# Kernel tuning notes

Measured on AMD Instinct MI355X. Metric: run time of the kernel, lower is better.

Reference implementation:

```python
import jax, jax.numpy as jnp
import numpy as np

BLOCK = 64  # bitsandbytes 4-bit blocksize
OUT, IN = 4096, 4096
# NF4 codebook (bitsandbytes values)
NF4_CODE = np.array([
    -1.0, -0.6961928009986877, -0.5250730514526367, -0.39491748809814453,
    -0.28444138169288635, -0.18477343022823334, -0.09105003625154495, 0.0,
    0.07958029955625534, 0.16093020141124725, 0.24611230194568634,
    0.33791524171829224, 0.44070982933044434, 0.5626170039176941,
    0.7229568362236023, 1.0], dtype=np.float32)


def setup_inputs() -> dict:
    key = jax.random.key(0)
    k1, k2, k3 = jax.random.split(key, 3)
    x = jax.random.normal(k1, (8, 2048, IN), dtype=jnp.float32)
    qweight = jax.random.randint(k2, (OUT * IN,), 0, 16, dtype=jnp.int32)
    absmax = jax.random.uniform(k3, (OUT * IN // BLOCK,), dtype=jnp.float32)
    return {"x": x, "qweight": qweight, "absmax": absmax}


def reference(x, qweight, absmax):
    code = jnp.asarray(NF4_CODE)
    # dequantize: codebook lookup, then per-block absmax scaling
    w = code[qweight].reshape(-1, BLOCK) * absmax[:, None]  # [n_blocks, BLOCK]
    W = w.reshape(OUT, IN)                                   # [out, in]
    # linear: y = x @ W^T  (no bias: quantized_bias is None)
    return jnp.einsum('bsi,oi->bso', x, W)
```

## Files before the change

### kernel.cpp

```cpp
#include <hip/hip_runtime.h>
#include <hip/hip_bf16.h>
#include <stdint.h>

#define IN_DIM  4096
#define OUT_DIM 4096
#define M_DIM   16384
#define BK      64
#define NT      (IN_DIM / BK)

typedef float f32x4 __attribute__((ext_vector_type(4)));
typedef short bf16x8 __attribute__((ext_vector_type(8)));
typedef short bf16x4 __attribute__((ext_vector_type(4)));
typedef int   i32x4 __attribute__((ext_vector_type(4)));

__device__ __constant__ float NF4_CODE_D[16] = {
    -1.0f, -0.6961928009986877f, -0.5250730514526367f, -0.39491748809814453f,
    -0.28444138169288635f, -0.18477343022823334f, -0.09105003625154495f, 0.0f,
    0.07958029955625534f, 0.16093020141124725f, 0.24611230194568634f,
    0.33791524171829224f, 0.44070982933044434f, 0.5626170039176941f,
    0.7229568362236023f, 1.0f};

static __device__ __forceinline__ ushort f2bf(float f) {
  union { float f; uint32_t u; } v; v.f = f;
  uint32_t r = v.u + 0x7FFFu + ((v.u >> 16) & 1u);
  return (ushort)(r >> 16);
}

#define NB_W 8192
__global__ void prep(const float* __restrict__ x, const int* __restrict__ q,
                     const float* __restrict__ am, ushort* __restrict__ xb,
                     ushort* __restrict__ w) {
  if (blockIdx.x < NB_W) {
    __shared__ float code[16];
    if (threadIdx.x < 16) code[threadIdx.x] = NF4_CODE_D[threadIdx.x];
    __syncthreads();
    size_t t = (size_t)blockIdx.x * 256 + threadIdx.x;
    size_t base = t * 8;
    i32x4 qa = *(const i32x4*)(q + base);
    i32x4 qb = *(const i32x4*)(q + base + 4);
    float s = am[base >> 6];
    bf16x8 o;
    o[0] = (short)f2bf(code[qa[0] & 15] * s);
    o[1] = (short)f2bf(code[qa[1] & 15] * s);
    o[2] = (short)f2bf(code[qa[2] & 15] * s);
    o[3] = (short)f2bf(code[qa[3] & 15] * s);
    o[4] = (short)f2bf(code[qb[0] & 15] * s);
    o[5] = (short)f2bf(code[qb[1] & 15] * s);
    o[6] = (short)f2bf(code[qb[2] & 15] * s);
    o[7] = (short)f2bf(code[qb[3] & 15] * s);
    *(bf16x8*)(w + base) = o;
  } else {
    size_t t = (size_t)(blockIdx.x - NB_W) * 256 + threadIdx.x;
    size_t base = t * 8;
    f32x4 a = *(const f32x4*)(x + base);
    f32x4 b = *(const f32x4*)(x + base + 4);
    bf16x8 o;
    o[0] = (short)f2bf(a[0]); o[1] = (short)f2bf(a[1]);
    o[2] = (short)f2bf(a[2]); o[3] = (short)f2bf(a[3]);
    o[4] = (short)f2bf(b[0]); o[5] = (short)f2bf(b[1]);
    o[6] = (short)f2bf(b[2]); o[7] = (short)f2bf(b[3]);
    *(bf16x8*)(xb + base) = o;
  }
}

static __device__ __forceinline__ void llds16(const ushort* g, ushort* l) {
  __builtin_amdgcn_global_load_lds(
      (const __attribute__((address_space(1))) void*)g,
      (__attribute__((address_space(3))) void*)l, 16, 0, 0);
}

__global__ __launch_bounds__(512, 2) void gemm256(const ushort* __restrict__ Xb,
                                                  const ushort* __restrict__ W,
                                                  float* __restrict__ Y) {
  __shared__ ushort As[2][256 * BK];
  __shared__ ushort Bs[2][256 * BK];

  const int tid  = threadIdx.x;
  const int lane = tid & 63;
  const int wid  = tid >> 6;
  const int wr   = wid >> 2;
  const int wc   = wid & 3;
  const int l15  = lane & 15;
  const int kg   = lane >> 4;
  const int l7   = lane & 7;

  const int bid = blockIdx.x;
  const int wg  = (bid & 7) * 128 + (bid >> 3);
  const int tm  = wg >> 4;
  const int tn  = wg & 15;
  const size_t row0 = (size_t)tm * 256;
  const size_t col0 = (size_t)tn * 256;

  const int srow  = tid >> 3;
  const int scol8 = ((tid & 7) ^ (srow & 7)) * 8;
  const int wbase = wid << 9;

  f32x4  acc[8][4] = {};
  bf16x8 aA[4][2], aB[4][2], b0[2][2], b1[2][2];

#define BARX()  __builtin_amdgcn_s_barrier()
#define VMC(n)  asm volatile("s_waitcnt vmcnt(" #n ")" ::: "memory")
#define PRI1()  __builtin_amdgcn_s_setprio(1)
#define PRI0()  __builtin_amdgcn_s_setprio(0)

#define STAGE_A(kt, h, nb) do { \
    llds16(Xb + (row0 + (h)*128 +  0 + srow) * IN_DIM + (kt)*BK + scol8, \
           &As[nb][(h)*8192 +    0 + wbase]); \
    llds16(Xb + (row0 + (h)*128 + 64 + srow) * IN_DIM + (kt)*BK + scol8, \
           &As[nb][(h)*8192 + 4096 + wbase]); \
  } while (0)

#define STAGE_B(kt, h, nb) do { \
    llds16(W + (col0 + (h)*128 +  0 + srow) * IN_DIM + (kt)*BK + scol8, \
           &Bs[nb][(h)*8192 +    0 + wbase]); \
    llds16(W + (col0 + (h)*128 + 64 + srow) * IN_DIM + (kt)*BK + scol8, \
           &Bs[nb][(h)*8192 + 4096 + wbase]); \
  } while (0)

#define LDA_(dst, nb, mh) do { \
    _Pragma("unroll") for (int mi = 0; mi < 4; ++mi) \
    _Pragma("unroll") for (int ks = 0; ks < 2; ++ks) \
      dst[mi][ks] = *(const bf16x8*)&As[nb][((mh)*128 + wr*64 + mi*16 + l15) * BK \
                                            + (((ks*4 + kg) ^ l7) * 8)]; \
  } while (0)

#define LDB_(dst, nb, nh) do { \
    _Pragma("unroll") for (int ni = 0; ni < 2; ++ni) \
    _Pragma("unroll") for (int ks = 0; ks < 2; ++ks) \
      dst[ni][ks] = *(const bf16x8*)&Bs[nb][((nh)*128 + wc*32 + ni*16 + l15) * BK \
                                            + (((ks*4 + kg) ^ l7) * 8)]; \
  } while (0)

#define QUAD(mh, nh, aR, bR) do { PRI1(); \
    _Pragma("unroll") for (int mi = 0; mi < 4; ++mi) \
    _Pragma("unroll") for (int ni = 0; ni < 2; ++ni) \
    _Pragma("unroll") for (int ks = 0; ks < 2; ++ks) \
      acc[(mh)*4 + mi][(nh)*2 + ni] = __builtin_amdgcn_mfma_f32_16x16x32_bf16( \
          aR[mi][ks], bR[ni][ks], acc[(mh)*4 + mi][(nh)*2 + ni], 0, 0, 0); \
    PRI0(); } while (0)

  STAGE_A(0, 0, 0); STAGE_A(0, 1, 0);
  STAGE_B(0, 0, 0); STAGE_B(0, 1, 0);
  STAGE_A(1, 0, 1);
  VMC(2); BARX();
  LDA_(aA, 0, 0); LDB_(b0, 0, 0);

#pragma unroll 1
  for (int t = 0; t < NT - 1; ++t) {
    const int cur = t & 1, nxt = cur ^ 1;
    STAGE_A(t + 1, 1, nxt);
    VMC(4); BARX();
    LDB_(b1, cur, 1); LDA_(aB, cur, 1);
    QUAD(0, 0, aA, b0);
    STAGE_B(t + 1, 0, nxt);
    BARX();
    QUAD(0, 1, aA, b1);
    STAGE_B(t + 1, 1, nxt);
    BARX();
    QUAD(1, 1, aB, b1);
    if (t < NT - 2) {
      STAGE_A(t + 2, 0, cur);
      VMC(4);
    } else {
      VMC(2);
    }
    BARX();
    QUAD(1, 0, aB, b0);
    LDA_(aA, nxt, 0); LDB_(b0, nxt, 0);
  }

  VMC(0); BARX();
  LDB_(b1, 1, 1); LDA_(aB, 1, 1);
  QUAD(0, 0, aA, b0);
  QUAD(0, 1, aA, b1);
  QUAD(1, 1, aB, b1);
  QUAD(1, 0, aB, b0);

#undef QUAD
#undef LDB_
#undef LDA_
#undef STAGE_B
#undef STAGE_A

  float* yb = Y + (row0 + wr * 64 + kg * 4) * OUT_DIM + col0 + wc * 32 + l15;
#pragma unroll
  for (int mh = 0; mh < 2; ++mh)
#pragma unroll
    for (int mi = 0; mi < 4; ++mi)
#pragma unroll
      for (int nh = 0; nh < 2; ++nh)
#pragma unroll
        for (int ni = 0; ni < 2; ++ni)
#pragma unroll
          for (int v = 0; v < 4; ++v)
            yb[(size_t)(mh * 128 + mi * 16 + v) * OUT_DIM + nh * 128 + ni * 16] =
                acc[mh * 4 + mi][nh * 2 + ni][v];
}

__global__ void gemm_fb(const float* __restrict__ X, const ushort* __restrict__ W,
                        float* __restrict__ Y) {
  __shared__ ushort Af[128 * 64];
  __shared__ ushort Bf[128 * 64];
  const int tid  = threadIdx.x;
  const int lane = tid & 63;
  const int wid  = tid >> 6;
  const int wr   = wid >> 1, wc = wid & 1;
  const int bid  = blockIdx.x;
  const int tm   = bid / 32, tn = bid % 32;
  const size_t row0 = (size_t)tm * 128, col0 = (size_t)tn * 128;
  f32x4 acc[4][4] = {};
  const int arow = lane & 15, kgrp = lane >> 4;
  const int srow = lane >> 3, scol = (lane & 7) * 8;
  for (int k0 = 0; k0 < IN_DIM; k0 += 64) {
    f32x4 r[8];
#pragma unroll
    for (int i = 0; i < 8; ++i)
      r[i] = *(const f32x4*)(X + (row0 + i * 16 + (tid >> 4)) * IN_DIM + k0 + (tid & 15) * 4);
#pragma unroll
    for (int i = 0; i < 8; ++i) {
      bf16x4 o;
      o[0] = (short)f2bf(r[i][0]); o[1] = (short)f2bf(r[i][1]);
      o[2] = (short)f2bf(r[i][2]); o[3] = (short)f2bf(r[i][3]);
      *(bf16x4*)&Af[(i * 16 + (tid >> 4)) * 64 + (tid & 15) * 4] = o;
    }
#pragma unroll
    for (int i = 0; i < 4; ++i) {
      const int c = wid * 4 + i;
      llds16(W + (col0 + c * 8 + srow) * IN_DIM + k0 + scol, Bf + c * 512);
    }
    __syncthreads();
#pragma unroll
    for (int ks = 0; ks < 2; ++ks) {
      bf16x8 a[4], b[4];
#pragma unroll
      for (int m = 0; m < 4; ++m)
        a[m] = *(const bf16x8*)&Af[(wr * 64 + m * 16 + arow) * 64 + ks * 32 + kgrp * 8];
#pragma unroll
      for (int n = 0; n < 4; ++n)
        b[n] = *(const bf16x8*)&Bf[(wc * 64 + n * 16 + arow) * 64 + ks * 32 + kgrp * 8];
#pragma unroll
      for (int m = 0; m < 4; ++m)
#pragma unroll
        for (int n = 0; n < 4; ++n)
          acc[m][n] = __builtin_amdgcn_mfma_f32_16x16x32_bf16(a[m], b[n], acc[m][n], 0, 0, 0);
    }
    __syncthreads();
  }
  float* yb = Y + (row0 + wr * 64) * OUT_DIM + col0 + wc * 64;
  const int crow = (lane >> 4) * 4, ccol = lane & 15;
#pragma unroll
  for (int m = 0; m < 4; ++m)
#pragma unroll
    for (int n = 0; n < 4; ++n)
#pragma unroll
      for (int v = 0; v < 4; ++v)
        yb[(size_t)(m * 16 + crow + v) * OUT_DIM + n * 16 + ccol] = acc[m][n][v];
}

extern "C" void kernel_launch(void* const* d_in, const int* in_sizes, int n_in,
                              void* d_out, int out_size, void* d_ws, size_t ws_size,
                              hipStream_t stream) {
  const float* x  = (const float*)d_in[0];
  const int*   q  = (const int*)d_in[1];
  const float* am = (const float*)d_in[2];
  float* y = (float*)d_out;

  ushort* w = (ushort*)d_ws;
  const size_t WB = (size_t)OUT_DIM * IN_DIM * sizeof(ushort);
  const size_t XB = (size_t)M_DIM * IN_DIM * sizeof(ushort);

  if (ws_size >= WB + XB) {
    ushort* xb = (ushort*)((char*)d_ws + WB);
    const int nb = NB_W + (int)((size_t)M_DIM * IN_DIM / 8 / 256);
    prep<<<nb, 256, 0, stream>>>(x, q, am, xb, w);
    gemm256<<<(M_DIM / 256) * (OUT_DIM / 256), 512, 0, stream>>>(xb, w, y);
  } else {
    prep<<<NB_W, 256, 0, stream>>>(x, q, am, nullptr, w);
    gemm_fb<<<(M_DIM / 128) * (OUT_DIM / 128), 256, 0, stream>>>(x, w, y);
  }
}
```

Measured before the change: 584.5 us.

## Load B operand directly from global into registers, dropping LDS staging for W

Removes the shared-memory double buffer for the weight tile. Each wave now reads its B fragments straight from global memory into registers, and the vmcnt waits are adjusted to match. This halves LDS usage and cuts LDS write and read traffic for B. In exchange, B tiles are no longer shared between waves, so global and L2 traffic for W rises, and the direct loads add latency on the MFMA critical path. The vmcnt accounting also looks fragile, because the register loads now count toward the same counter.

```diff
diff --git a/kernel.cpp b/kernel.cpp
--- a/kernel.cpp
+++ b/kernel.cpp
@@ -73,7 +73,6 @@
                                                   const ushort* __restrict__ W,
                                                   float* __restrict__ Y) {
   __shared__ ushort As[2][256 * BK];
-  __shared__ ushort Bs[2][256 * BK];
 
   const int tid  = threadIdx.x;
   const int lane = tid & 63;
@@ -110,13 +109,6 @@
            &As[nb][(h)*8192 + 4096 + wbase]); \
   } while (0)
 
-#define STAGE_B(kt, h, nb) do { \
-    llds16(W + (col0 + (h)*128 +  0 + srow) * IN_DIM + (kt)*BK + scol8, \
-           &Bs[nb][(h)*8192 +    0 + wbase]); \
-    llds16(W + (col0 + (h)*128 + 64 + srow) * IN_DIM + (kt)*BK + scol8, \
-           &Bs[nb][(h)*8192 + 4096 + wbase]); \
-  } while (0)
-
 #define LDA_(dst, nb, mh) do { \
     _Pragma("unroll") for (int mi = 0; mi < 4; ++mi) \
     _Pragma("unroll") for (int ks = 0; ks < 2; ++ks) \
@@ -124,11 +116,11 @@
                                             + (((ks*4 + kg) ^ l7) * 8)]; \
   } while (0)
 
-#define LDB_(dst, nb, nh) do { \
+#define GLBB_(dst, kt, nh) do { \
     _Pragma("unroll") for (int ni = 0; ni < 2; ++ni) \
     _Pragma("unroll") for (int ks = 0; ks < 2; ++ks) \
-      dst[ni][ks] = *(const bf16x8*)&Bs[nb][((nh)*128 + wc*32 + ni*16 + l15) * BK \
-                                            + (((ks*4 + kg) ^ l7) * 8)]; \
+      dst[ni][ks] = *(const bf16x8*)&W[(col0 + (nh)*128 + wc*32 + ni*16 + l15) \
+                                       * (size_t)IN_DIM + (kt)*BK + (ks*4 + kg)*8]; \
   } while (0)
 
 #define QUAD(mh, nh, aR, bR) do { PRI1(); \
@@ -139,47 +131,46 @@
           aR[mi][ks], bR[ni][ks], acc[(mh)*4 + mi][(nh)*2 + ni], 0, 0, 0); \
     PRI0(); } while (0)
 
+  GLBB_(b0, 0, 0);
   STAGE_A(0, 0, 0); STAGE_A(0, 1, 0);
-  STAGE_B(0, 0, 0); STAGE_B(0, 1, 0);
   STAGE_A(1, 0, 1);
   VMC(2); BARX();
-  LDA_(aA, 0, 0); LDB_(b0, 0, 0);
+  LDA_(aA, 0, 0);
 
 #pragma unroll 1
   for (int t = 0; t < NT - 1; ++t) {
     const int cur = t & 1, nxt = cur ^ 1;
+    GLBB_(b1, t, 1);
     STAGE_A(t + 1, 1, nxt);
-    VMC(4); BARX();
-    LDB_(b1, cur, 1); LDA_(aB, cur, 1);
+    BARX();
+    LDA_(aB, cur, 1);
     QUAD(0, 0, aA, b0);
-    STAGE_B(t + 1, 0, nxt);
     BARX();
     QUAD(0, 1, aA, b1);
-    STAGE_B(t + 1, 1, nxt);
     BARX();
     QUAD(1, 1, aB, b1);
     if (t < NT - 2) {
       STAGE_A(t + 2, 0, cur);
-      VMC(4);
+      VMC(2);
     } else {
-      VMC(2);
+      VMC(0);
     }
     BARX();
     QUAD(1, 0, aB, b0);
-    LDA_(aA, nxt, 0); LDB_(b0, nxt, 0);
-  }
-
-  VMC(0); BARX();
-  LDB_(b1, 1, 1); LDA_(aB, 1, 1);
+    GLBB_(b0, t + 1, 0);
+    LDA_(aA, nxt, 0);
+  }
+
+  GLBB_(b1, NT - 1, 1);
+  LDA_(aB, 1, 1);
   QUAD(0, 0, aA, b0);
   QUAD(0, 1, aA, b1);
   QUAD(1, 1, aB, b1);
   QUAD(1, 0, aB, b0);
 
 #undef QUAD
-#undef LDB_
+#undef GLBB_
 #undef LDA_
-#undef STAGE_B
 #undef STAGE_A
 
   float* yb = Y + (row0 + wr * 64 + kg * 4) * OUT_DIM + col0 + wc * 32 + l15;
```

Result: slower. 918.5 us (+57.1%).
